# Kernel optimization log

Hardware: AMD Instinct MI355X
Metric: run time of the kernel (lower is better)

## Reference

```python
import jax, jax.numpy as jnp
import numpy as np

N = 50000   # nodes per graph batch
E = 800000  # directed edges
B = 64      # graphs


def gat_layer(x, src, dst, W, a_s, a_d, bias, heads, concat):
    # PyG GATConv (eval mode): linear (no bias), self-loops, LeakyReLU(0.2) logits,
    # softmax over incoming edges per target node, weighted sum, concat/mean heads, +bias.
    n = x.shape[0]
    c = a_s.shape[-1]
    xl = (x @ W).reshape(n, heads, c)          # [N,H,C]
    loops = jnp.arange(n)
    src = jnp.concatenate([src, loops])
    dst = jnp.concatenate([dst, loops])
    e_src = jnp.sum(xl * a_s[None], axis=-1)   # [N,H]
    e_dst = jnp.sum(xl * a_d[None], axis=-1)   # [N,H]
    e = jax.nn.leaky_relu(e_src[src] + e_dst[dst], 0.2)  # [E+N,H]
    emax = jax.ops.segment_max(e, dst, num_segments=n)
    emax = jnp.where(jnp.isfinite(emax), emax, 0.0)
    ex = jnp.exp(e - emax[dst])
    denom = jax.ops.segment_sum(ex, dst, num_segments=n)
    alpha = ex / jnp.maximum(denom[dst], 1e-16)           # [E+N,H]
    out = jax.ops.segment_sum(alpha[:, :, None] * xl[src], dst, num_segments=n)  # [N,H,C]
    out = out.reshape(n, heads * c) if concat else out.mean(axis=1)
    return out + bias


def branch_trunk(x, ei, batch, W1, a1s, a1d, b1, W2, a2s, a2d, b2, M1w, M1b, M2w, M2b):
    h = jax.nn.elu(gat_layer(x, ei[0], ei[1], W1, a1s, a1d, b1, 2, True))
    h = jax.nn.elu(gat_layer(h, ei[0], ei[1], W2, a2s, a2d, b2, 1, True))
    cnt = jax.ops.segment_sum(jnp.ones((x.shape[0],), h.dtype), batch, num_segments=B)
    pooled = jax.ops.segment_sum(h, batch, num_segments=B) / jnp.maximum(cnt, 1.0)[:, None]
    h = jax.nn.relu(pooled @ M1w + M1b)
    return h @ M2w + M2b


def setup_inputs() -> dict:
    key = jax.random.key(0)
    ks = jax.random.split(key, 32)
    rn = lambda k, s, sc=0.1: jax.random.normal(k, s, jnp.float32) * sc
    inp = {}
    i = 0
    for tag in ('b', 't'):
        inp[f'x_{tag}'] = jax.random.normal(ks[i], (N, 2), jnp.float32); i += 1
        inp[f'edge_index_{tag}'] = jax.random.randint(ks[i], (2, E), 0, N); i += 1
        inp[f'batch_{tag}'] = jnp.sort(jax.random.randint(ks[i], (N,), 0, B)); i += 1
        inp[f'W1_{tag}'] = rn(ks[i], (2, 128)); i += 1
        inp[f'a1s_{tag}'] = rn(ks[i], (2, 64)); i += 1
        inp[f'a1d_{tag}'] = rn(ks[i], (2, 64)); i += 1
        inp[f'b1_{tag}'] = jnp.zeros((128,), jnp.float32)
        inp[f'W2_{tag}'] = rn(ks[i], (128, 64)); i += 1
        inp[f'a2s_{tag}'] = rn(ks[i], (1, 64)); i += 1
        inp[f'a2d_{tag}'] = rn(ks[i], (1, 64)); i += 1
        inp[f'b2_{tag}'] = jnp.zeros((64,), jnp.float32)
        inp[f'M1w_{tag}'] = rn(ks[i], (64, 64)); i += 1
        inp[f'M1b_{tag}'] = jnp.zeros((64,), jnp.float32)
        inp[f'M2w_{tag}'] = rn(ks[i], (64, 64)); i += 1
        inp[f'M2b_{tag}'] = jnp.zeros((64,), jnp.float32)
    inp['Fw1'] = rn(ks[i], (64, 64)); i += 1
    inp['Fb1'] = jnp.zeros((64,), jnp.float32)
    inp['Fw2'] = rn(ks[i], (64, 2)); i += 1
    inp['Fb2'] = jnp.zeros((2,), jnp.float32)
    return inp


def reference(x_b, edge_index_b, batch_b, W1_b, a1s_b, a1d_b, b1_b, W2_b, a2s_b, a2d_b, b2_b,
              M1w_b, M1b_b, M2w_b, M2b_b,
              x_t, edge_index_t, batch_t, W1_t, a1s_t, a1d_t, b1_t, W2_t, a2s_t, a2d_t, b2_t,
              M1w_t, M1b_t, M2w_t, M2b_t,
              Fw1, Fb1, Fw2, Fb2):
    branch = branch_trunk(x_b, edge_index_b, batch_b, W1_b, a1s_b, a1d_b, b1_b,
                          W2_b, a2s_b, a2d_b, b2_b, M1w_b, M1b_b, M2w_b, M2b_b)
    trunk = branch_trunk(x_t, edge_index_t, batch_t, W1_t, a1s_t, a1d_t, b1_t,
                         W2_t, a2s_t, a2d_t, b2_t, M1w_t, M1b_t, M2w_t, M2b_t)
    combined = branch * trunk
    h = jax.nn.relu(combined @ Fw1 + Fb1)
    return jnp.tanh(h @ Fw2 + Fb2)  # [B,2]
```

## Files before the change

kernel.cpp:

```cpp
#include <hip/hip_runtime.h>
#include <math.h>


#define BSH 9
#define CHUNK 4096
#define ARENA 12288
#define LOG2E 1.44269504088896f

using short8v = __attribute__((ext_vector_type(8))) short;
using f32x4  = __attribute__((ext_vector_type(4))) float;

__device__ __forceinline__ float leaky02(float x){ return fmaxf(x, 0.2f * x); }
__device__ __forceinline__ float elu1(float x){ return x > 0.f ? x : expm1f(x); }
__device__ __forceinline__ unsigned f2bf(float a){
    unsigned u = __float_as_uint(a);
    return (u + 0x7FFFu + ((u >> 16) & 1u)) >> 16;
}
__device__ __forceinline__ unsigned packbf(float a, float b){ return f2bf(a) | (f2bf(b) << 16); }
__device__ __forceinline__ float bflo(unsigned p){ return __uint_as_float(p << 16); }
__device__ __forceinline__ float bfhi(unsigned p){ return __uint_as_float(p & 0xFFFF0000u); }
__device__ __forceinline__ float bfs(unsigned short s){ return __uint_as_float(((unsigned)s) << 16); }

__device__ __forceinline__ int wave_incl_scan(int v, int lane){
    #pragma unroll
    for (int d = 1; d < 64; d <<= 1){ int u = __shfl_up(v, (unsigned)d, 64); if (lane >= d) v += u; }
    return v;
}

__global__ __launch_bounds__(256) void preb_kernel(
    const float* __restrict__ xb, const float* __restrict__ xt,
    const float* __restrict__ W1b, const float* __restrict__ W1t,
    const float* __restrict__ a1sb, const float* __restrict__ a1st,
    const float* __restrict__ a1db, const float* __restrict__ a1dt,
    const int* __restrict__ eib, const int* __restrict__ eit,
    const float* __restrict__ W2b, const float* __restrict__ W2t,
    float* __restrict__ es1, float* __restrict__ ed1,
    int* __restrict__ bcur, unsigned* __restrict__ epair,
    unsigned short* __restrict__ w2T, float* __restrict__ pooled,
    int N, int E, int NB, int nodeBlocks, int histBlocks){
    int bid = blockIdx.x;
    int tid = threadIdx.x;
    __shared__ int hist[128], gpos[128];
    __shared__ int slots[CHUNK];
    if (bid < 2 * histBlocks){
        int br = (bid >= histBlocks) ? 1 : 0;
        int cb = bid - br * histBlocks;
        const int* ei = br ? eit : eib;
        int start = cb * CHUNK;
        int cnt = min(CHUNK, E - start);
        for (int i = tid; i < 128; i += 256) hist[i] = 0;
        __syncthreads();
        const int* dstp = ei + E + start;
        const int* srcp = ei + start;
        for (int li = tid; li < cnt; li += 256){
            int b = dstp[li] >> BSH;
            slots[li] = atomicAdd(&hist[b], 1);
        }
        __syncthreads();
        if (tid < NB){
            int h0 = hist[tid];
            gpos[tid] = (h0 > 0) ? atomicAdd(&bcur[br * NB + tid], h0) : 0;
        }
        __syncthreads();
        unsigned* ep = epair + (size_t)br * NB * ARENA;
        for (int li = tid; li < cnt; li += 256){
            int d = dstp[li];
            int b = d >> BSH;
            ep[(size_t)b * ARENA + gpos[b] + slots[li]] =
                ((unsigned)srcp[li] << BSH) | (unsigned)(d & ((1 << BSH) - 1));
        }
        return;
    }
    bid -= 2 * histBlocks;
    if (bid >= 2 * nodeBlocks){
        int xb2 = bid - 2 * nodeBlocks;
        if (xb2 < 2){
            const float* W2 = xb2 ? W2t : W2b;
            for (int i = tid; i < 8192; i += 256){
                int c = i >> 7, k = i & 127;
                w2T[xb2 * 8192 + i] = (unsigned short)f2bf(W2[k * 64 + c]);
            }
        } else {
            for (int i = tid; i < 8192; i += 256) pooled[i] = 0.f;
        }
        return;
    }
    int br = (bid >= nodeBlocks) ? 1 : 0;
    int nb = bid - br * nodeBlocks;
    int n = (nb << 2) + (tid >> 6);
    int lane = tid & 63;
    if (n >= N) return;
    const float* x   = br ? xt   : xb;
    const float* W1  = br ? W1t  : W1b;
    const float* a1s = br ? a1st : a1sb;
    const float* a1d = br ? a1dt : a1db;
    float2 xv = ((const float2*)x)[n];
    float2 w0 = ((const float2*)W1)[lane];
    float2 w1 = ((const float2*)(W1 + 128))[lane];
    float xla = xv.x * w0.x + xv.y * w1.x;
    float xlb = xv.x * w0.y + xv.y * w1.y;
    float2 as = ((const float2*)a1s)[lane];
    float2 ad = ((const float2*)a1d)[lane];
    float ps = xla * as.x + xlb * as.y;
    float pd = xla * ad.x + xlb * ad.y;
    #pragma unroll
    for (int m = 16; m >= 1; m >>= 1){ ps += __shfl_xor(ps, m, 64); pd += __shfl_xor(pd, m, 64); }
    if ((lane & 31) == 0){
        int h = lane >> 5;
        es1[(size_t)br * N * 2 + n * 2 + h] = LOG2E * ps;
        ed1[(size_t)br * N * 2 + n * 2 + h] = LOG2E * pd;
    }
}

__global__ __launch_bounds__(256) void csr_kernel(
    const int* __restrict__ bcur, const unsigned* __restrict__ epair,
    int* __restrict__ rs, int* __restrict__ csr, int N, int E, int NB){
    int bid = blockIdx.x;
    int br = (bid >= NB) ? 1 : 0;
    int b = bid - br * NB;
    __shared__ int base2[128];
    __shared__ int deg[512], st[512];
    int tid = threadIdx.x, lane = tid & 63, wid = tid >> 6;
    if (wid == 0){
        int b0 = (lane < NB) ? bcur[br * NB + lane] : 0;
        int b1 = (64 + lane < NB) ? bcur[br * NB + 64 + lane] : 0;
        int g0 = wave_incl_scan(b0, lane); int gt = __shfl(g0, 63, 64);
        int g1 = wave_incl_scan(b1, lane);
        base2[lane] = g0 - b0; base2[64 + lane] = gt + g1 - b1;
    }
    for (int i = tid; i < 512; i += 256) deg[i] = 0;
    __syncthreads();
    int ebase = base2[b];
    int ecnt = bcur[br * NB + b];
    int n0 = b << BSH;
    int nodes = min(512, N - n0);
    const unsigned* ep = epair + ((size_t)br * NB + b) * ARENA;
    for (int i = tid; i < ecnt; i += 256) atomicAdd(&deg[ep[i] & 511u], 1);
    __syncthreads();
    if (wid == 0){
        int carry = 0;
        #pragma unroll
        for (int c = 0; c < 8; ++c){
            int v = deg[c * 64 + lane];
            int s = wave_incl_scan(v, lane);
            st[c * 64 + lane] = carry + s - v;
            carry += __shfl(s, 63, 64);
        }
    }
    __syncthreads();
    int* rsb = rs + (size_t)br * (N + 1);
    for (int i = tid; i < nodes; i += 256) rsb[n0 + i] = ebase + st[i];
    if (b == NB - 1 && tid == 0) rsb[N] = ebase + ecnt;
    for (int i = tid; i < 512; i += 256) deg[i] = st[i];
    __syncthreads();
    int* csrb = csr + (size_t)br * E + ebase;
    for (int i = tid; i < ecnt; i += 256){
        unsigned p = ep[i];
        int pos = atomicAdd(&deg[p & 511u], 1);
        csrb[pos] = (int)(p >> BSH);
    }
}

__global__ __launch_bounds__(256) void a1f2_kernel(
    const float* __restrict__ xB, const float* __restrict__ xT,
    const float* __restrict__ es1, const float* __restrict__ ed1,
    const int* __restrict__ csr, const int* __restrict__ rs,
    const float* __restrict__ W1b, const float* __restrict__ W1t,
    const float* __restrict__ b1b, const float* __restrict__ b1t,
    const unsigned short* __restrict__ w2T,
    const float* __restrict__ a2sb, const float* __restrict__ a2st,
    const float* __restrict__ a2db, const float* __restrict__ a2dt,
    unsigned short* __restrict__ xl2h, float* __restrict__ es2, float* __restrict__ ed2,
    int N, int E){
    int bid = blockIdx.x;
    int br = bid & 1;
    int n0 = (bid >> 1) << 5;
    const float* x  = br ? xT : xB;
    const float* es = es1 + (size_t)br * N * 2;
    const float* ed = ed1 + (size_t)br * N * 2;
    const int* cs = csr + (size_t)br * E;
    const int* rsb = rs + (size_t)br * (N + 1);
    const float* W1 = br ? W1t : W1b;
    const float* b1 = br ? b1t : b1b;
    const float* a2s = br ? a2st : a2sb;
    const float* a2d = br ? a2dt : a2db;

    __shared__ float sacc[32][6];
    __shared__ unsigned hl[32][68];
    __shared__ float psa[4][32], pda[4][32];
    int tid = threadIdx.x, lane = tid & 63, w = tid >> 6;
    int g = lane >> 3, sl = lane & 7;
    int row = w * 8 + g;
    int n = n0 + row;
    bool valid = n < N;

    float2 edv = ((const float2*)ed)[valid ? n : 0];
    int beg = 0, end = 0;
    if (valid){ beg = rsb[n]; end = rsb[n + 1]; }
    float d0 = 0.f, s0x = 0.f, s0y = 0.f, d1 = 0.f, s1x = 0.f, s1y = 0.f;
    if (valid && sl == 0){
        float2 xv = ((const float2*)x)[n];
        float2 ev = ((const float2*)es)[n];
        float w0 = exp2f(leaky02(ev.x + edv.x));
        float w1 = exp2f(leaky02(ev.y + edv.y));
        d0 = w0; s0x = w0 * xv.x; s0y = w0 * xv.y;
        d1 = w1; s1x = w1 * xv.x; s1y = w1 * xv.y;
    }
    for (int j = beg + sl; j < end; j += 8){
        int s = cs[j];
        float2 xv = ((const float2*)x)[s];
        float2 ev = ((const float2*)es)[s];
        float w0 = exp2f(leaky02(ev.x + edv.x));
        float w1 = exp2f(leaky02(ev.y + edv.y));
        d0 += w0; s0x += w0 * xv.x; s0y += w0 * xv.y;
        d1 += w1; s1x += w1 * xv.x; s1y += w1 * xv.y;
    }
    #pragma unroll
    for (int m = 1; m < 8; m <<= 1){
        d0  += __shfl_xor(d0, m, 64);
        s0x += __shfl_xor(s0x, m, 64);
        s0y += __shfl_xor(s0y, m, 64);
        d1  += __shfl_xor(d1, m, 64);
        s1x += __shfl_xor(s1x, m, 64);
        s1y += __shfl_xor(s1y, m, 64);
    }
    if (sl == 0){
        sacc[row][0] = d0; sacc[row][1] = s0x; sacc[row][2] = s0y;
        sacc[row][3] = d1; sacc[row][4] = s1x; sacc[row][5] = s1y;
    }
    __syncthreads();

    int h = lane >> 5;
    float2 w0c = ((const float2*)W1)[lane];
    float2 w1c = ((const float2*)(W1 + 128))[lane];
    float b1lo = b1[lane * 2], b1hi = b1[lane * 2 + 1];
    #pragma unroll
    for (int nn = 0; nn < 8; ++nn){
        int r2 = w * 8 + nn;
        int nr = n0 + r2;
        float dinv = 1.f / sacc[r2][3 * h];
        float sx = sacc[r2][3 * h + 1], sy = sacc[r2][3 * h + 2];
        float va = (sx * w0c.x + sy * w1c.x) * dinv + b1lo;
        float vb = (sx * w0c.y + sy * w1c.y) * dinv + b1hi;
        hl[r2][lane] = (nr < N) ? packbf(elu1(va), elu1(vb)) : 0u;
    }

    int lr = lane & 15, lq = lane >> 4;
    const unsigned short* wtp = w2T + br * 8192 + (w * 16 + lr) * 128 + lq * 8;
    short8v bf0 = *(const short8v*)(wtp);
    short8v bf1 = *(const short8v*)(wtp + 32);
    short8v bf2 = *(const short8v*)(wtp + 64);
    short8v bf3 = *(const short8v*)(wtp + 96);
    float a2sv = a2s[w * 16 + lr];
    float a2dv = a2d[w * 16 + lr];
    __syncthreads();
    #pragma unroll
    for (int rt = 0; rt < 2; ++rt){
        int rb = rt << 4;
        f32x4 ac = {0.f, 0.f, 0.f, 0.f};
        ac = __builtin_amdgcn_mfma_f32_16x16x32_bf16(*(const short8v*)&hl[rb + lr][lq * 4], bf0, ac, 0, 0, 0);
        ac = __builtin_amdgcn_mfma_f32_16x16x32_bf16(*(const short8v*)&hl[rb + lr][16 + lq * 4], bf1, ac, 0, 0, 0);
        ac = __builtin_amdgcn_mfma_f32_16x16x32_bf16(*(const short8v*)&hl[rb + lr][32 + lq * 4], bf2, ac, 0, 0, 0);
        ac = __builtin_amdgcn_mfma_f32_16x16x32_bf16(*(const short8v*)&hl[rb + lr][48 + lq * 4], bf3, ac, 0, 0, 0);
        #pragma unroll
        for (int reg = 0; reg < 4; ++reg){
            int r = rb + lq * 4 + reg;
            int nr = n0 + r;
            float v = ac[reg];
            if (nr < N)
                xl2h[((size_t)br * N + nr) * 64 + w * 16 + lr] = (unsigned short)f2bf(v);
            float ps = v * a2sv, pd = v * a2dv;
            ps += __shfl_xor(ps, 1, 64); ps += __shfl_xor(ps, 2, 64);
            ps += __shfl_xor(ps, 4, 64); ps += __shfl_xor(ps, 8, 64);
            pd += __shfl_xor(pd, 1, 64); pd += __shfl_xor(pd, 2, 64);
            pd += __shfl_xor(pd, 4, 64); pd += __shfl_xor(pd, 8, 64);
            if (lr == 0){ psa[w][r] = ps; pda[w][r] = pd; }
        }
    }
    __syncthreads();
    if (tid < 32){
        int nr = n0 + tid;
        if (nr < N)
            es2[(size_t)br * N + nr] = LOG2E * (psa[0][tid] + psa[1][tid] + psa[2][tid] + psa[3][tid]);
    } else if (tid < 64){
        int r = tid - 32;
        int nr = n0 + r;
        if (nr < N)
            ed2[(size_t)br * N + nr] = LOG2E * (pda[0][r] + pda[1][r] + pda[2][r] + pda[3][r]);
    }
}

__global__ __launch_bounds__(256) void a2pl_kernel(
    const unsigned short* __restrict__ xl2h, const float* __restrict__ es2, const float* __restrict__ ed2,
    const int* __restrict__ csr, const int* __restrict__ rs,
    const float* __restrict__ b2b, const float* __restrict__ b2t,
    const int* __restrict__ batchb, const int* __restrict__ batcht,
    float* __restrict__ pooled, int N, int E){
    int bid = blockIdx.x;
    int br = bid & 1;
    int tid = threadIdx.x, lane = tid & 63, w = tid >> 6;
    int n = ((bid >> 1) << 2) + w;
    const unsigned short* xlt = xl2h + (size_t)br * N * 64;
    const float* es = es2 + (size_t)br * N;
    const float* ed = ed2 + (size_t)br * N;
    const int* cs = csr + (size_t)br * E;
    const int* rsb = rs + (size_t)br * (N + 1);
    const float* b2 = br ? b2t : b2b;
    const int* batch = br ? batcht : batchb;
    float hv = 0.f;
    int g = -1;
    if (n < N){
        float edn = ed[n];
        float wself = exp2f(leaky02(es[n] + edn));
        float denom = wself;
        float acc = wself * bfs(xlt[(unsigned)(n * 64) + lane]);
        int beg = rsb[n];
        int end = rsb[n + 1];
        for (int base = beg; base < end; base += 64){
            int cnt = min(64, end - base);
            int myidx = cs[base + min(lane, cnt - 1)];
            float wmine = (lane < cnt) ? exp2f(leaky02(es[myidx] + edn)) : 0.f;
            float ws = wmine;
            #pragma unroll
            for (int m = 1; m < 64; m <<= 1) ws += __shfl_xor(ws, m, 64);
            denom += ws;
            int cntR = (cnt + 7) & ~7;
            for (int q = 0; q < cntR; q += 8){
                #pragma unroll
                for (int qq = 0; qq < 8; ++qq){
                    int s = __builtin_amdgcn_readlane(myidx, q + qq);
                    float wq = __uint_as_float(
                        __builtin_amdgcn_readlane(__float_as_uint(wmine), q + qq));
                    float v = bfs(xlt[(unsigned)(s * 64) + lane]);
                    acc += wq * v;
                }
            }
        }
        hv = elu1(acc / denom + b2[lane]);
        g = batch[n];
    }
    __shared__ float red[4][64];
    __shared__ int gid[4];
    red[w][lane] = hv;
    if (lane == 0) gid[w] = g;
    __syncthreads();
    if (w == 0){
        int g0 = gid[0], g1 = gid[1], g2 = gid[2], g3 = gid[3];
        float* pb = pooled + (size_t)br * 4096;
        if (g0 >= 0 && g0 == g1 && g1 == g2 && g2 == g3){
            float s = (red[0][lane] + red[1][lane]) + (red[2][lane] + red[3][lane]);
            atomicAdd(&pb[g0 * 64 + lane], s);
        } else {
            #pragma unroll
            for (int q = 0; q < 4; ++q)
                if (gid[q] >= 0) atomicAdd(&pb[gid[q] * 64 + lane], red[q][lane]);
        }
    }
}

__global__ __launch_bounds__(1024) void tail_kernel(
    const float* __restrict__ pooled,
    const int* __restrict__ batchb, const int* __restrict__ batcht,
    const float* __restrict__ M1wb, const float* __restrict__ M1bb,
    const float* __restrict__ M2wb, const float* __restrict__ M2bb,
    const float* __restrict__ M1wt, const float* __restrict__ M1bt,
    const float* __restrict__ M2wt, const float* __restrict__ M2bt,
    const float* __restrict__ Fw1, const float* __restrict__ Fb1,
    const float* __restrict__ Fw2, const float* __restrict__ Fb2,
    float* __restrict__ out, int N){
    __shared__ float P[8192];
    __shared__ float H[8192];
    __shared__ float cl[128];
    int t = threadIdx.x;
    if (t < 128){
        int br = t >> 6, g = t & 63;
        const int* batch = br ? batcht : batchb;
        int lo = 0, hi = N;
        while (lo < hi){ int mid = (lo + hi) >> 1; if (batch[mid] < g) lo = mid + 1; else hi = mid; }
        int beg = lo;
        hi = N;
        while (lo < hi){ int mid = (lo + hi) >> 1; if (batch[mid] < g + 1) lo = mid + 1; else hi = mid; }
        cl[t] = (float)(lo - beg);
    }
    __syncthreads();
    for (int i = t; i < 8192; i += 1024)
        P[i] = pooled[i] / fmaxf(cl[i >> 6], 1.f);
    __syncthreads();
    for (int i = t; i < 8192; i += 1024){
        int br = i >> 12, r = (i >> 6) & 63, c = i & 63;
        const float* M1w = br ? M1wt : M1wb;
        const float* M1b = br ? M1bt : M1bb;
        float acc = M1b[c];
        int pb = (br << 12) + (r << 6);
        #pragma unroll 8
        for (int k = 0; k < 64; ++k) acc += P[pb + k] * M1w[(k << 6) + c];
        H[i] = fmaxf(acc, 0.f);
    }
    __syncthreads();
    for (int i = t; i < 8192; i += 1024){
        int br = i >> 12, r = (i >> 6) & 63, c = i & 63;
        const float* M2w = br ? M2wt : M2wb;
        const float* M2b = br ? M2bt : M2bb;
        float acc = M2b[c];
        int hb = (br << 12) + (r << 6);
        #pragma unroll 8
        for (int k = 0; k < 64; ++k) acc += H[hb + k] * M2w[(k << 6) + c];
        P[i] = acc;
    }
    __syncthreads();
    for (int i = t; i < 4096; i += 1024) H[i] = P[i] * P[4096 + i];
    __syncthreads();
    for (int i = t; i < 4096; i += 1024){
        int r = i >> 6, c = i & 63;
        float acc = Fb1[c];
        #pragma unroll 8
        for (int k = 0; k < 64; ++k) acc += H[(r << 6) + k] * Fw1[(k << 6) + c];
        P[i] = fmaxf(acc, 0.f);
    }
    __syncthreads();
    if (t < 128){
        int r = t >> 1, jc = t & 1;
        float acc = Fb2[jc];
        #pragma unroll 8
        for (int k = 0; k < 64; ++k) acc += P[(r << 6) + k] * Fw2[k * 2 + jc];
        out[t] = tanhf(acc);
    }
}

extern "C" void kernel_launch(void* const* d_in, const int* in_sizes, int n_in,
                              void* d_out, int out_size, void* d_ws, size_t ws_size,
                              hipStream_t stream){
    const int N = in_sizes[0] / 2;
    const int E = in_sizes[1] / 2;
    const int NB = (N + 511) >> BSH;

    char* ws = (char*)d_ws;
    size_t off = 0;
    auto alloc = [&](size_t bytes) -> char* {
        char* p = ws + off;
        off += (bytes + 255) & ~(size_t)255;
        return p;
    };
    unsigned short* XL2h = (unsigned short*)alloc((size_t)2 * N * 64 * 2);
    float* ES1 = (float*)alloc((size_t)2 * N * 2 * 4);
    float* ED1 = (float*)alloc((size_t)2 * N * 2 * 4);
    float* ES2 = (float*)alloc((size_t)2 * N * 4);
    float* ED2 = (float*)alloc((size_t)2 * N * 4);
    int* RS  = (int*)alloc((size_t)2 * (N + 1) * 4);
    int* CSR = (int*)alloc((size_t)2 * E * 4);
    int* BCUR = (int*)alloc((size_t)2 * NB * 4);
    float* POOLED = (float*)alloc(8192 * 4);
    unsigned short* W2T = (unsigned short*)alloc(2 * 8192 * 2);
    unsigned* EPAIR = (unsigned*)XL2h;

    const float* xb   = (const float*)d_in[0];
    const int*   eib  = (const int*)  d_in[1];
    const int*   batchb = (const int*)d_in[2];
    const float* W1b  = (const float*)d_in[3];
    const float* a1sb = (const float*)d_in[4];
    const float* a1db = (const float*)d_in[5];
    const float* b1b  = (const float*)d_in[6];
    const float* W2b  = (const float*)d_in[7];
    const float* a2sb = (const float*)d_in[8];
    const float* a2db = (const float*)d_in[9];
    const float* b2b  = (const float*)d_in[10];
    const float* M1wb = (const float*)d_in[11];
    const float* M1bb = (const float*)d_in[12];
    const float* M2wb = (const float*)d_in[13];
    const float* M2bb = (const float*)d_in[14];
    const float* xt   = (const float*)d_in[15];
    const int*   eit  = (const int*)  d_in[16];
    const int*   batcht = (const int*)d_in[17];
    const float* W1t  = (const float*)d_in[18];
    const float* a1st = (const float*)d_in[19];
    const float* a1dt = (const float*)d_in[20];
    const float* b1t  = (const float*)d_in[21];
    const float* W2t  = (const float*)d_in[22];
    const float* a2st = (const float*)d_in[23];
    const float* a2dt = (const float*)d_in[24];
    const float* b2t  = (const float*)d_in[25];
    const float* M1wt = (const float*)d_in[26];
    const float* M1bt = (const float*)d_in[27];
    const float* M2wt = (const float*)d_in[28];
    const float* M2bt = (const float*)d_in[29];
    const float* Fw1  = (const float*)d_in[30];
    const float* Fb1  = (const float*)d_in[31];
    const float* Fw2  = (const float*)d_in[32];
    const float* Fb2  = (const float*)d_in[33];

    const int nodeBlocks = (N + 3) / 4;
    const int histBlocks = (E + CHUNK - 1) / CHUNK;
    const int tilesPer   = (N + 31) / 32;

    hipMemsetAsync(BCUR, 0, (size_t)2 * NB * 4, stream);
    preb_kernel<<<2 * histBlocks + 2 * nodeBlocks + 3, 256, 0, stream>>>(
        xb, xt, W1b, W1t, a1sb, a1st, a1db, a1dt, eib, eit, W2b, W2t,
        ES1, ED1, BCUR, EPAIR, W2T, POOLED, N, E, NB, nodeBlocks, histBlocks);
    csr_kernel<<<2 * NB, 256, 0, stream>>>(BCUR, EPAIR, RS, CSR, N, E, NB);
    a1f2_kernel<<<2 * tilesPer, 256, 0, stream>>>(
        xb, xt, ES1, ED1, CSR, RS, W1b, W1t, b1b, b1t, W2T,
        a2sb, a2st, a2db, a2dt, XL2h, ES2, ED2, N, E);
    a2pl_kernel<<<2 * nodeBlocks, 256, 0, stream>>>(
        XL2h, ES2, ED2, CSR, RS, b2b, b2t, batchb, batcht, POOLED, N, E);
    tail_kernel<<<1, 1024, 0, stream>>>(POOLED, batchb, batcht,
        M1wb, M1bb, M2wb, M2bb, M1wt, M1bt, M2wt, M2bt,
        Fw1, Fb1, Fw2, Fb2, (float*)d_out, N);
}
```

Measured before the change: 218.2 us.

## Fold layer-1 attention vectors into W1 and recompute logits from raw x

Because the input has only two features, the layer-1 source and destination logits are linear in x. The change precomputes eight folded coefficients (W1 times a1s and a1d, scaled by log2 e) per branch and has the aggregation kernel compute logits directly from x. This removes the per-node logit pass and the ES1/ED1 gather traffic in exchange for a few extra FMAs per edge. Separately, the layer-2 gather loop is unrolled to 16 with loads batched before the FMAs to expose more memory parallelism, and the batch index load is hoisted earlier.

```diff
diff --git a/kernel.cpp b/kernel.cpp
--- a/kernel.cpp
+++ b/kernel.cpp
@@ -28,16 +28,15 @@
 }
 
 __global__ __launch_bounds__(256) void preb_kernel(
-    const float* __restrict__ xb, const float* __restrict__ xt,
     const float* __restrict__ W1b, const float* __restrict__ W1t,
     const float* __restrict__ a1sb, const float* __restrict__ a1st,
     const float* __restrict__ a1db, const float* __restrict__ a1dt,
     const int* __restrict__ eib, const int* __restrict__ eit,
     const float* __restrict__ W2b, const float* __restrict__ W2t,
-    float* __restrict__ es1, float* __restrict__ ed1,
     int* __restrict__ bcur, unsigned* __restrict__ epair,
-    unsigned short* __restrict__ w2T, float* __restrict__ pooled,
-    int N, int E, int NB, int nodeBlocks, int histBlocks){
+    unsigned short* __restrict__ w2T, float* __restrict__ alph,
+    float* __restrict__ pooled,
+    int N, int E, int NB, int histBlocks){
     int bid = blockIdx.x;
     int tid = threadIdx.x;
     __shared__ int hist[128], gpos[128];
@@ -72,43 +71,29 @@
         return;
     }
     bid -= 2 * histBlocks;
-    if (bid >= 2 * nodeBlocks){
-        int xb2 = bid - 2 * nodeBlocks;
-        if (xb2 < 2){
-            const float* W2 = xb2 ? W2t : W2b;
-            for (int i = tid; i < 8192; i += 256){
-                int c = i >> 7, k = i & 127;
-                w2T[xb2 * 8192 + i] = (unsigned short)f2bf(W2[k * 64 + c]);
+    if (bid < 2){
+        int br = bid;
+        const float* W2 = br ? W2t : W2b;
+        for (int i = tid; i < 8192; i += 256){
+            int c = i >> 7, k = i & 127;
+            w2T[br * 8192 + i] = (unsigned short)f2bf(W2[k * 64 + c]);
+        }
+        if (tid < 64){
+            const float* W1  = br ? W1t  : W1b;
+            const float* a1s = br ? a1st : a1sb;
+            const float* a1d = br ? a1dt : a1db;
+            int lane = tid;
+            for (int k = 0; k < 8; ++k){
+                int sd = k >> 2, h = (k >> 1) & 1, xr = k & 1;
+                const float* av = sd ? a1d : a1s;
+                float p = W1[xr * 128 + h * 64 + lane] * av[h * 64 + lane];
+                #pragma unroll
+                for (int m = 32; m >= 1; m >>= 1) p += __shfl_xor(p, m, 64);
+                if (lane == 0) alph[br * 8 + k] = LOG2E * p;
             }
-        } else {
-            for (int i = tid; i < 8192; i += 256) pooled[i] = 0.f;
-        }
-        return;
-    }
-    int br = (bid >= nodeBlocks) ? 1 : 0;
-    int nb = bid - br * nodeBlocks;
-    int n = (nb << 2) + (tid >> 6);
-    int lane = tid & 63;
-    if (n >= N) return;
-    const float* x   = br ? xt   : xb;
-    const float* W1  = br ? W1t  : W1b;
-    const float* a1s = br ? a1st : a1sb;
-    const float* a1d = br ? a1dt : a1db;
-    float2 xv = ((const float2*)x)[n];
-    float2 w0 = ((const float2*)W1)[lane];
-    float2 w1 = ((const float2*)(W1 + 128))[lane];
-    float xla = xv.x * w0.x + xv.y * w1.x;
-    float xlb = xv.x * w0.y + xv.y * w1.y;
-    float2 as = ((const float2*)a1s)[lane];
-    float2 ad = ((const float2*)a1d)[lane];
-    float ps = xla * as.x + xlb * as.y;
-    float pd = xla * ad.x + xlb * ad.y;
-    #pragma unroll
-    for (int m = 16; m >= 1; m >>= 1){ ps += __shfl_xor(ps, m, 64); pd += __shfl_xor(pd, m, 64); }
-    if ((lane & 31) == 0){
-        int h = lane >> 5;
-        es1[(size_t)br * N * 2 + n * 2 + h] = LOG2E * ps;
-        ed1[(size_t)br * N * 2 + n * 2 + h] = LOG2E * pd;
+        }
+    } else {
+        for (int i = tid; i < 8192; i += 256) pooled[i] = 0.f;
     }
 }
 
@@ -163,7 +148,7 @@
 
 __global__ __launch_bounds__(256) void a1f2_kernel(
     const float* __restrict__ xB, const float* __restrict__ xT,
-    const float* __restrict__ es1, const float* __restrict__ ed1,
+    const float* __restrict__ alph,
     const int* __restrict__ csr, const int* __restrict__ rs,
     const float* __restrict__ W1b, const float* __restrict__ W1t,
     const float* __restrict__ b1b, const float* __restrict__ b1t,
@@ -176,14 +161,15 @@
     int br = bid & 1;
     int n0 = (bid >> 1) << 5;
     const float* x  = br ? xT : xB;
-    const float* es = es1 + (size_t)br * N * 2;
-    const float* ed = ed1 + (size_t)br * N * 2;
     const int* cs = csr + (size_t)br * E;
     const int* rsb = rs + (size_t)br * (N + 1);
     const float* W1 = br ? W1t : W1b;
     const float* b1 = br ? b1t : b1b;
     const float* a2s = br ? a2st : a2sb;
     const float* a2d = br ? a2dt : a2db;
+    const float* al = alph + br * 8;
+    float as0x = al[0], as0y = al[1], as1x = al[2], as1y = al[3];
+    float ad0x = al[4], ad0y = al[5], ad1x = al[6], ad1y = al[7];
 
     __shared__ float sacc[32][6];
     __shared__ unsigned hl[32][68];
@@ -194,24 +180,27 @@
     int n = n0 + row;
     bool valid = n < N;
 
-    float2 edv = ((const float2*)ed)[valid ? n : 0];
+    float2 xn = ((const float2*)x)[valid ? n : 0];
+    float edv0 = ad0x * xn.x + ad0y * xn.y;
+    float edv1 = ad1x * xn.x + ad1y * xn.y;
     int beg = 0, end = 0;
     if (valid){ beg = rsb[n]; end = rsb[n + 1]; }
     float d0 = 0.f, s0x = 0.f, s0y = 0.f, d1 = 0.f, s1x = 0.f, s1y = 0.f;
     if (valid && sl == 0){
-        float2 xv = ((const float2*)x)[n];
-        float2 ev = ((const float2*)es)[n];
-        float w0 = exp2f(leaky02(ev.x + edv.x));
-        float w1 = exp2f(leaky02(ev.y + edv.y));
-        d0 = w0; s0x = w0 * xv.x; s0y = w0 * xv.y;
-        d1 = w1; s1x = w1 * xv.x; s1y = w1 * xv.y;
+        float e0 = as0x * xn.x + as0y * xn.y;
+        float e1 = as1x * xn.x + as1y * xn.y;
+        float w0 = exp2f(leaky02(e0 + edv0));
+        float w1 = exp2f(leaky02(e1 + edv1));
+        d0 = w0; s0x = w0 * xn.x; s0y = w0 * xn.y;
+        d1 = w1; s1x = w1 * xn.x; s1y = w1 * xn.y;
     }
     for (int j = beg + sl; j < end; j += 8){
         int s = cs[j];
         float2 xv = ((const float2*)x)[s];
-        float2 ev = ((const float2*)es)[s];
-        float w0 = exp2f(leaky02(ev.x + edv.x));
-        float w1 = exp2f(leaky02(ev.y + edv.y));
+        float e0 = as0x * xv.x + as0y * xv.y;
+        float e1 = as1x * xv.x + as1y * xv.y;
+        float w0 = exp2f(leaky02(e0 + edv0));
+        float w1 = exp2f(leaky02(e1 + edv1));
         d0 += w0; s0x += w0 * xv.x; s0y += w0 * xv.y;
         d1 += w1; s1x += w1 * xv.x; s1y += w1 * xv.y;
     }
@@ -310,6 +299,7 @@
     float hv = 0.f;
     int g = -1;
     if (n < N){
+        g = batch[n];
         float edn = ed[n];
         float wself = exp2f(leaky02(es[n] + edn));
         float denom = wself;
@@ -324,20 +314,23 @@
             #pragma unroll
             for (int m = 1; m < 64; m <<= 1) ws += __shfl_xor(ws, m, 64);
             denom += ws;
-            int cntR = (cnt + 7) & ~7;
-            for (int q = 0; q < cntR; q += 8){
+            int cntR = (cnt + 15) & ~15;
+            for (int q0 = 0; q0 < cntR; q0 += 16){
+                float vv[16];
                 #pragma unroll
-                for (int qq = 0; qq < 8; ++qq){
-                    int s = __builtin_amdgcn_readlane(myidx, q + qq);
+                for (int qq = 0; qq < 16; ++qq){
+                    int s = __builtin_amdgcn_readlane(myidx, q0 + qq);
+                    vv[qq] = bfs(xlt[(unsigned)(s * 64) + lane]);
+                }
+                #pragma unroll
+                for (int qq = 0; qq < 16; ++qq){
                     float wq = __uint_as_float(
-                        __builtin_amdgcn_readlane(__float_as_uint(wmine), q + qq));
-                    float v = bfs(xlt[(unsigned)(s * 64) + lane]);
-                    acc += wq * v;
+                        __builtin_amdgcn_readlane(__float_as_uint(wmine), q0 + qq));
+                    acc += wq * vv[qq];
                 }
             }
         }
         hv = elu1(acc / denom + b2[lane]);
-        g = batch[n];
     }
     __shared__ float red[4][64];
     __shared__ int gid[4];
@@ -442,8 +435,6 @@
         return p;
     };
     unsigned short* XL2h = (unsigned short*)alloc((size_t)2 * N * 64 * 2);
-    float* ES1 = (float*)alloc((size_t)2 * N * 2 * 4);
-    float* ED1 = (float*)alloc((size_t)2 * N * 2 * 4);
     float* ES2 = (float*)alloc((size_t)2 * N * 4);
     float* ED2 = (float*)alloc((size_t)2 * N * 4);
     int* RS  = (int*)alloc((size_t)2 * (N + 1) * 4);
@@ -451,6 +442,7 @@
     int* BCUR = (int*)alloc((size_t)2 * NB * 4);
     float* POOLED = (float*)alloc(8192 * 4);
     unsigned short* W2T = (unsigned short*)alloc(2 * 8192 * 2);
+    float* ALPH = (float*)alloc(16 * 4);
     unsigned* EPAIR = (unsigned*)XL2h;
 
     const float* xb   = (const float*)d_in[0];
@@ -493,12 +485,12 @@
     const int tilesPer   = (N + 31) / 32;
 
     hipMemsetAsync(BCUR, 0, (size_t)2 * NB * 4, stream);
-    preb_kernel<<<2 * histBlocks + 2 * nodeBlocks + 3, 256, 0, stream>>>(
-        xb, xt, W1b, W1t, a1sb, a1st, a1db, a1dt, eib, eit, W2b, W2t,
-        ES1, ED1, BCUR, EPAIR, W2T, POOLED, N, E, NB, nodeBlocks, histBlocks);
+    preb_kernel<<<2 * histBlocks + 3, 256, 0, stream>>>(
+        W1b, W1t, a1sb, a1st, a1db, a1dt, eib, eit, W2b, W2t,
+        BCUR, EPAIR, W2T, ALPH, POOLED, N, E, NB, histBlocks);
     csr_kernel<<<2 * NB, 256, 0, stream>>>(BCUR, EPAIR, RS, CSR, N, E, NB);
     a1f2_kernel<<<2 * tilesPer, 256, 0, stream>>>(
-        xb, xt, ES1, ED1, CSR, RS, W1b, W1t, b1b, b1t, W2T,
+        xb, xt, ALPH, CSR, RS, W1b, W1t, b1b, b1t, W2T,
         a2sb, a2st, a2db, a2dt, XL2h, ES2, ED2, N, E);
     a2pl_kernel<<<2 * nodeBlocks, 256, 0, stream>>>(
         XL2h, ES2, ED2, CSR, RS, b2b, b2t, batchb, batcht, POOLED, N, E);
```

New measurement: 202.4 us. -7.3%, faster.
